# Optimization experiments

Hardware: AMD Instinct MI355X
Metric: run time of the kernel (lower is better)

## Reference

```python
import jax, jax.numpy as jnp
import numpy as np

N = 100000      # nodes
E = 1600000     # edges (avg degree 16)
IN = 128        # in_channels
H = 128         # hidden_channels
EPS = 1e-5      # BatchNorm eps


def setup_inputs() -> dict:
    key = jax.random.key(0)
    ks = jax.random.split(key, 10)
    x = jax.random.normal(ks[0], (N, IN), jnp.float32)
    edge_index = jax.random.randint(ks[1], (2, E), 0, N, dtype=jnp.int32)

    def lin(k, i, o):
        return jax.random.normal(k, (i, o), jnp.float32) * (1.0 / np.sqrt(i))

    d2 = 2 * H
    return {
        "x": x, "edge_index": edge_index,
        # SAGEConv 1: 128 -> 128
        "w1l": lin(ks[2], IN, H), "w1r": lin(ks[3], IN, H), "b1": jnp.zeros((H,), jnp.float32),
        "g1": jnp.ones((H,), jnp.float32), "be1": jnp.zeros((H,), jnp.float32),
        "m1": jnp.zeros((H,), jnp.float32), "v1": jnp.ones((H,), jnp.float32),
        # SAGEConv 2: 128 -> 256
        "w2l": lin(ks[4], H, d2), "w2r": lin(ks[5], H, d2), "b2": jnp.zeros((d2,), jnp.float32),
        "g2": jnp.ones((d2,), jnp.float32), "be2": jnp.zeros((d2,), jnp.float32),
        "m2": jnp.zeros((d2,), jnp.float32), "v2": jnp.ones((d2,), jnp.float32),
        # SAGEConv 3: 256 -> 256
        "w3l": lin(ks[6], d2, d2), "w3r": lin(ks[7], d2, d2), "b3": jnp.zeros((d2,), jnp.float32),
        "g3": jnp.ones((d2,), jnp.float32), "be3": jnp.zeros((d2,), jnp.float32),
        "m3": jnp.zeros((d2,), jnp.float32), "v3": jnp.ones((d2,), jnp.float32),
    }


def _sage_conv(x, src, dst, wl, wr, b):
    # PyG SAGEConv (mean aggr): out = mean_{j in N(i)} x_j @ W_l + x_i @ W_r + b
    agg = jax.ops.segment_sum(x[src], dst, num_segments=N)          # [N, d_in]
    deg = jax.ops.segment_sum(jnp.ones((src.shape[0],), x.dtype), dst, num_segments=N)
    mean = agg / jnp.maximum(deg, 1.0)[:, None]
    return mean @ wl + x @ wr + b


def _bn(x, g, b, m, v):
    # BatchNorm1d in eval mode (running stats); dropout is a no-op in eval
    return (x - m) * jax.lax.rsqrt(v + EPS) * g + b


def reference(x, edge_index,
              w1l, w1r, b1, g1, be1, m1, v1,
              w2l, w2r, b2, g2, be2, m2, v2,
              w3l, w3r, b3, g3, be3, m3, v3):
    src, dst = edge_index[0], edge_index[1]
    h = _bn(jax.nn.relu(_sage_conv(x, src, dst, w1l, w1r, b1)), g1, be1, m1, v1)
    h = _bn(jax.nn.relu(_sage_conv(h, src, dst, w2l, w2r, b2)), g2, be2, m2, v2)
    h = _bn(jax.nn.relu(_sage_conv(h, src, dst, w3l, w3r, b3)), g3, be3, m3, v3)
    return h  # [N, 2*H]
```

## Files before the change

### kernel.cpp

```cpp
#include <hip/hip_runtime.h>

#define NNODES 100000
#define NEDGES 1600000
#define EPSV 1e-5f

#define NB   391
#define BCAP 4608
#define EPB  4096

typedef __attribute__((ext_vector_type(8))) short bf16x8;
typedef __attribute__((ext_vector_type(4))) float f32x4;

#if defined(__has_builtin)
#  if __has_builtin(__builtin_amdgcn_cvt_pk_f32_fp8) && __has_builtin(__builtin_amdgcn_cvt_pk_fp8_f32)
#    define HAS_FP8_CVT 1
#  endif
#endif
#ifndef HAS_FP8_CVT
#  define HAS_FP8_CVT 0
#endif

__device__ __forceinline__ ushort f2bf(float f) {
    union { float f; uint u; } c; c.f = f;
    uint u = c.u;
    return (ushort)((u + 0x7fffu + ((u >> 16) & 1u)) >> 16);
}
__device__ __forceinline__ uint pack2(float f0, float f1) {
    return (uint)f2bf(f0) | ((uint)f2bf(f1) << 16);
}

#if !HAS_FP8_CVT
__device__ __forceinline__ float fp8_dec1(uint b) {
    uint e = (b >> 3) & 0xFu, m = b & 7u, s = b >> 7;
    union { uint u; float f; } c;
    c.u = e ? ((s << 31) | ((e + 120u) << 23) | (m << 20)) : (s << 31);
    return c.f;
}
__device__ __forceinline__ uint fp8_enc1(float x) {
    union { float f; uint u; } c; c.f = x;
    uint u = c.u, s = u >> 31;
    float ax = fabsf(x);
    if (ax < 0.015625f) return s << 7;
    if (ax > 448.0f)    return (s << 7) | 0x7Eu;
    u = u + 0x7FFFFu + ((u >> 20) & 1u);
    uint e = ((u >> 23) & 0xFFu) - 120u;
    uint m = (u >> 20) & 7u;
    if (e > 15u) return (s << 7) | 0x7Eu;
    return (s << 7) | (e << 3) | m;
}
#endif

__device__ __forceinline__ void accf8(float* a, uint2 v) {
#if HAS_FP8_CVT
    auto p0 = __builtin_amdgcn_cvt_pk_f32_fp8((int)v.x, false);
    auto p1 = __builtin_amdgcn_cvt_pk_f32_fp8((int)v.x, true);
    auto p2 = __builtin_amdgcn_cvt_pk_f32_fp8((int)v.y, false);
    auto p3 = __builtin_amdgcn_cvt_pk_f32_fp8((int)v.y, true);
    a[0] += p0[0]; a[1] += p0[1]; a[2] += p1[0]; a[3] += p1[1];
    a[4] += p2[0]; a[5] += p2[1]; a[6] += p3[0]; a[7] += p3[1];
#else
    a[0] += fp8_dec1(v.x & 0xFFu);         a[1] += fp8_dec1((v.x >> 8) & 0xFFu);
    a[2] += fp8_dec1((v.x >> 16) & 0xFFu); a[3] += fp8_dec1(v.x >> 24);
    a[4] += fp8_dec1(v.y & 0xFFu);         a[5] += fp8_dec1((v.y >> 8) & 0xFFu);
    a[6] += fp8_dec1((v.y >> 16) & 0xFFu); a[7] += fp8_dec1(v.y >> 24);
#endif
}

__device__ __forceinline__ uint f2fp8(float f) {
#if HAS_FP8_CVT
    return ((uint)__builtin_amdgcn_cvt_pk_fp8_f32(f, f, 0, false)) & 0xFFu;
#else
    return fp8_enc1(f);
#endif
}

__device__ __forceinline__ uint packf8_4(float f0, float f1, float f2, float f3) {
#if HAS_FP8_CVT
    int r = 0;
    r = __builtin_amdgcn_cvt_pk_fp8_f32(f0, f1, r, false);
    r = __builtin_amdgcn_cvt_pk_fp8_f32(f2, f3, r, true);
    return (uint)r;
#else
    return fp8_enc1(f0) | (fp8_enc1(f1) << 8) | (fp8_enc1(f2) << 16) | (fp8_enc1(f3) << 24);
#endif
}

__global__ __launch_bounds__(256) void part_kernel(
    const int* __restrict__ src, const int* __restrict__ dst,
    int* __restrict__ cursor, uint2* __restrict__ pairs, int E)
{
    __shared__ int lcnt[NB];
    __shared__ int lbase[NB];
    const int t = threadIdx.x;
    for (int i = t; i < NB; i += 256) lcnt[i] = 0;
    __syncthreads();

    const int base = blockIdx.x * EPB;
    const int lim  = min(base + EPB, E);

    for (int e = base + t; e < lim; e += 256)
        atomicAdd(&lcnt[((unsigned)dst[e]) >> 8], 1);
    __syncthreads();

    for (int i = t; i < NB; i += 256) {
        int c = lcnt[i];
        lbase[i] = c ? atomicAdd(&cursor[i], c) : 0;
        lcnt[i] = 0;
    }
    __syncthreads();

    for (int e = base + t; e < lim; e += 256) {
        int d = dst[e];
        int b = ((unsigned)d) >> 8;
        int p = lbase[b] + atomicAdd(&lcnt[b], 1);
        if (p < BCAP) pairs[(size_t)b * BCAP + p] = make_uint2((uint)src[e], (uint)d);
    }
}

__global__ __launch_bounds__(512) void bscan_kernel(const int* __restrict__ cursor,
                                                    int* __restrict__ colBase)
{
    __shared__ int s[512];
    int t = threadIdx.x;
    int v = (t < NB) ? min(cursor[t], BCAP) : 0;
    s[t] = v;
    __syncthreads();
    #pragma unroll
    for (int off = 1; off < 512; off <<= 1) {
        int a = (t >= off) ? s[t - off] : 0;
        __syncthreads();
        s[t] += a;
        __syncthreads();
    }
    if (t < NB) colBase[t] = s[t] - v;
}

__global__ __launch_bounds__(256) void csr_fin_kernel(
    const uint2* __restrict__ pairs, const int* __restrict__ cursor,
    const int* __restrict__ colBase, int* __restrict__ cnt,
    int* __restrict__ rptr, int* __restrict__ col, int n)
{
    __shared__ int lcnt[256];
    __shared__ int lofs[256];
    const int b = blockIdx.x;
    const int t = threadIdx.x;
    const int ecnt  = min(cursor[b], BCAP);
    const int cbase = colBase[b];
    const uint2* __restrict__ pp = pairs + (size_t)b * BCAP;

    lcnt[t] = 0;
    __syncthreads();
    for (int e = t; e < ecnt; e += 256)
        atomicAdd(&lcnt[pp[e].y & 255u], 1);
    __syncthreads();

    const int v = lcnt[t];
    lofs[t] = v;
    __syncthreads();
    #pragma unroll
    for (int off = 1; off < 256; off <<= 1) {
        int a = (t >= off) ? lofs[t - off] : 0;
        __syncthreads();
        lofs[t] += a;
        __syncthreads();
    }
    const int excl = lofs[t] - v;

    const int node = (b << 8) + t;
    if (node < n) {
        cnt[node]  = v;
        rptr[node] = cbase + excl + v;
    }
    __syncthreads();
    lcnt[t] = excl;
    __syncthreads();

    for (int e = t; e < ecnt; e += 256) {
        uint2 pr = pp[e];
        int p = cbase + atomicAdd(&lcnt[pr.y & 255u], 1);
        col[p] = (int)pr.x;
    }
}

__global__ void cvt_x_kernel(const float* __restrict__ in, ushort* __restrict__ outb,
                             unsigned char* __restrict__ out8, int n4) {
    int i = blockIdx.x * blockDim.x + threadIdx.x;
    if (i < n4) {
        float4 v = ((const float4*)in)[i];
        ushort4 o;
        o.x = f2bf(v.x); o.y = f2bf(v.y); o.z = f2bf(v.z); o.w = f2bf(v.w);
        ((ushort4*)outb)[i] = o;
        ((uint*)out8)[i] = packf8_4(v.x, v.y, v.z, v.w);
    }
}

__global__ void wT_all_kernel(
    const float* __restrict__ w1l, const float* __restrict__ w1r,
    const float* __restrict__ w2l, const float* __restrict__ w2r,
    const float* __restrict__ w3l, const float* __restrict__ w3r,
    ushort* __restrict__ t1l, ushort* __restrict__ t1r,
    ushort* __restrict__ t2l, ushort* __restrict__ t2r,
    ushort* __restrict__ t3l, ushort* __restrict__ t3r)
{
    int idx = blockIdx.x * blockDim.x + threadIdx.x;
    const float* w; ushort* wt; int K, Nout, i;
    if      (idx <  16384) { w = w1l; wt = t1l; K = 128; Nout = 128; i = idx; }
    else if (idx <  32768) { w = w1r; wt = t1r; K = 128; Nout = 128; i = idx - 16384; }
    else if (idx <  65536) { w = w2l; wt = t2l; K = 128; Nout = 256; i = idx - 32768; }
    else if (idx <  98304) { w = w2r; wt = t2r; K = 128; Nout = 256; i = idx - 65536; }
    else if (idx < 163840) { w = w3l; wt = t3l; K = 256; Nout = 256; i = idx - 98304; }
    else if (idx < 229376) { w = w3r; wt = t3r; K = 256; Nout = 256; i = idx - 163840; }
    else return;
    int k = i / Nout, n = i - k * Nout;
    wt[(size_t)n * K + k] = f2bf(w[i]);
}

template<int D>
__global__ __launch_bounds__(256) void gather_f8(
    const unsigned char* __restrict__ x, const int* __restrict__ rptr,
    const int* __restrict__ cnt, const int* __restrict__ col,
    ushort* __restrict__ agg, int n)
{
    constexpr int TPN = D / 8;
    constexpr int NPB = 256 / TPN;
    const int node = blockIdx.x * NPB + threadIdx.x / TPN;
    const int lane = threadIdx.x % TPN;
    if (node >= n) return;

    const int c   = cnt[node];
    const int end = rptr[node];
    const uint2* __restrict__ xp = (const uint2*)x + lane;

    float a[8] = {};
    int e = end - c;
    for (; e + 7 < end; e += 8) {
        int s0 = col[e],     s1 = col[e + 1], s2 = col[e + 2], s3 = col[e + 3];
        int s4 = col[e + 4], s5 = col[e + 5], s6 = col[e + 6], s7 = col[e + 7];
        uint2 v0 = xp[(size_t)s0 * TPN];
        uint2 v1 = xp[(size_t)s1 * TPN];
        uint2 v2 = xp[(size_t)s2 * TPN];
        uint2 v3 = xp[(size_t)s3 * TPN];
        uint2 v4 = xp[(size_t)s4 * TPN];
        uint2 v5 = xp[(size_t)s5 * TPN];
        uint2 v6 = xp[(size_t)s6 * TPN];
        uint2 v7 = xp[(size_t)s7 * TPN];
        accf8(a, v0); accf8(a, v1); accf8(a, v2); accf8(a, v3);
        accf8(a, v4); accf8(a, v5); accf8(a, v6); accf8(a, v7);
    }
    for (; e + 1 < end; e += 2) {
        uint2 v0 = xp[(size_t)col[e] * TPN];
        uint2 v1 = xp[(size_t)col[e + 1] * TPN];
        accf8(a, v0); accf8(a, v1);
    }
    if (e < end) accf8(a, xp[(size_t)col[e] * TPN]);

    const float inv = 1.0f / fmaxf((float)c, 1.0f);
    uint4 o;
    o.x = pack2(a[0] * inv, a[1] * inv);
    o.y = pack2(a[2] * inv, a[3] * inv);
    o.z = pack2(a[4] * inv, a[5] * inv);
    o.w = pack2(a[6] * inv, a[7] * inv);
    ((uint4*)agg)[(size_t)node * TPN + lane] = o;
}

template<int DIN, int DOUT, bool OUTF32, bool WRITE8>
__global__ __launch_bounds__(256) void mfma_layer(
    const ushort* __restrict__ xin, const ushort* __restrict__ agg,
    const ushort* __restrict__ wlT, const ushort* __restrict__ wrT,
    const float* __restrict__ bias, const float* __restrict__ gamma,
    const float* __restrict__ beta, const float* __restrict__ rmean,
    const float* __restrict__ rvar, void* __restrict__ outp,
    unsigned char* __restrict__ out8, int M)
{
    constexpr int BM = 128, BN = 128, BK = 32;
    constexpr int LDA = BK + 8;
    __shared__ ushort As[BM * LDA];
    __shared__ ushort Bs[BN * LDA];

    const int tid  = threadIdx.x;
    const int lane = tid & 63;
    const int wid  = tid >> 6;
    const int wm   = (wid & 1) * 64;
    const int wn   = (wid >> 1) * 64;
    const int lr   = lane & 15;
    const int quad = lane >> 4;

    const int row0 = blockIdx.x * BM;
    const int col0 = blockIdx.y * BN;

    f32x4 acc[4][4] = {};

    const int s_row  = tid >> 2;
    const int s_koff = (tid & 3) * 8;

    #pragma unroll
    for (int phase = 0; phase < 2; ++phase) {
        const ushort* __restrict__ A = phase ? xin : agg;
        const ushort* __restrict__ W = phase ? wrT : wlT;

        for (int k0 = 0; k0 < DIN; k0 += BK) {
            int gr0 = row0 + s_row;       gr0 = gr0 < M ? gr0 : M - 1;
            int gr1 = row0 + s_row + 64;  gr1 = gr1 < M ? gr1 : M - 1;
            uint4 a0v = *(const uint4*)(A + (size_t)gr0 * DIN + k0 + s_koff);
            uint4 a1v = *(const uint4*)(A + (size_t)gr1 * DIN + k0 + s_koff);
            uint4 b0v = *(const uint4*)(W + (size_t)(col0 + s_row) * DIN + k0 + s_koff);
            uint4 b1v = *(const uint4*)(W + (size_t)(col0 + s_row + 64) * DIN + k0 + s_koff);

            __syncthreads();
            *(uint4*)&As[s_row * LDA + s_koff]        = a0v;
            *(uint4*)&As[(s_row + 64) * LDA + s_koff] = a1v;
            *(uint4*)&Bs[s_row * LDA + s_koff]        = b0v;
            *(uint4*)&Bs[(s_row + 64) * LDA + s_koff] = b1v;
            __syncthreads();

            bf16x8 af[4], bf[4];
            #pragma unroll
            for (int t = 0; t < 4; ++t) {
                af[t] = *(const bf16x8*)&As[(wm + t * 16 + lr) * LDA + quad * 8];
                bf[t] = *(const bf16x8*)&Bs[(wn + t * 16 + lr) * LDA + quad * 8];
            }
            #pragma unroll
            for (int mt = 0; mt < 4; ++mt)
                #pragma unroll
                for (int nt = 0; nt < 4; ++nt)
                    acc[mt][nt] = __builtin_amdgcn_mfma_f32_16x16x32_bf16(
                        af[mt], bf[nt], acc[mt][nt], 0, 0, 0);
        }
    }

    float bj[4], sj[4], mj[4], bej[4];
    #pragma unroll
    for (int nt = 0; nt < 4; ++nt) {
        int gc = col0 + wn + nt * 16 + lr;
        bj[nt]  = bias[gc];
        sj[nt]  = rsqrtf(rvar[gc] + EPSV) * gamma[gc];
        mj[nt]  = rmean[gc];
        bej[nt] = beta[gc];
    }
    #pragma unroll
    for (int mt = 0; mt < 4; ++mt) {
        #pragma unroll
        for (int r = 0; r < 4; ++r) {
            int grow = row0 + wm + mt * 16 + quad * 4 + r;
            if (grow < M) {
                #pragma unroll
                for (int nt = 0; nt < 4; ++nt) {
                    int gc = col0 + wn + nt * 16 + lr;
                    float h = acc[mt][nt][r] + bj[nt];
                    h = fmaxf(h, 0.0f);
                    h = (h - mj[nt]) * sj[nt] + bej[nt];
                    if (OUTF32) ((float*)outp)[(size_t)grow * DOUT + gc] = h;
                    else        ((ushort*)outp)[(size_t)grow * DOUT + gc] = f2bf(h);
                    if (WRITE8) out8[(size_t)grow * DOUT + gc] = (unsigned char)f2fp8(h);
                }
            }
        }
    }
}

extern "C" void kernel_launch(void* const* d_in, const int* in_sizes, int n_in,
                              void* d_out, int out_size, void* d_ws, size_t ws_size,
                              hipStream_t stream) {
    const int N = NNODES;
    const int E = NEDGES;

    const float* x   = (const float*)d_in[0];
    const int*   ei  = (const int*)d_in[1];
    const int*   src = ei;
    const int*   dst = ei + E;

    const float* w1l = (const float*)d_in[2];
    const float* w1r = (const float*)d_in[3];
    const float* b1  = (const float*)d_in[4];
    const float* g1  = (const float*)d_in[5];
    const float* be1 = (const float*)d_in[6];
    const float* m1  = (const float*)d_in[7];
    const float* v1  = (const float*)d_in[8];

    const float* w2l = (const float*)d_in[9];
    const float* w2r = (const float*)d_in[10];
    const float* b2  = (const float*)d_in[11];
    const float* g2  = (const float*)d_in[12];
    const float* be2 = (const float*)d_in[13];
    const float* m2  = (const float*)d_in[14];
    const float* v2  = (const float*)d_in[15];

    const float* w3l = (const float*)d_in[16];
    const float* w3r = (const float*)d_in[17];
    const float* b3  = (const float*)d_in[18];
    const float* g3  = (const float*)d_in[19];
    const float* be3 = (const float*)d_in[20];
    const float* m3  = (const float*)d_in[21];
    const float* v3  = (const float*)d_in[22];

    float* out = (float*)d_out;

    char*   wp      = (char*)d_ws;
    int*    cnt     = (int*)wp;     wp += (size_t)N * sizeof(int);
    int*    rptr    = (int*)wp;     wp += (size_t)N * sizeof(int);
    int*    cursor  = (int*)wp;     wp += 512 * sizeof(int);
    int*    colBase = (int*)wp;     wp += 512 * sizeof(int);
    int*    col     = (int*)wp;     wp += (size_t)E * sizeof(int);
    uint2*  pairs   = (uint2*)wp;   wp += (size_t)NB * BCAP * sizeof(uint2);
    ushort* xbf     = (ushort*)wp;  wp += (size_t)N * 128 * sizeof(ushort);
    ushort* h1      = (ushort*)wp;  wp += (size_t)N * 128 * sizeof(ushort);
    ushort* h2      = (ushort*)wp;  wp += (size_t)N * 256 * sizeof(ushort);
    ushort* aggb    = (ushort*)wp;  wp += (size_t)N * 256 * sizeof(ushort);
    unsigned char* h2f8 = (unsigned char*)wp; wp += (size_t)N * 256;
    ushort* w1lT    = (ushort*)wp;  wp += 128 * 128 * sizeof(ushort);
    ushort* w1rT    = (ushort*)wp;  wp += 128 * 128 * sizeof(ushort);
    ushort* w2lT    = (ushort*)wp;  wp += 256 * 128 * sizeof(ushort);
    ushort* w2rT    = (ushort*)wp;  wp += 256 * 128 * sizeof(ushort);
    ushort* w3lT    = (ushort*)wp;  wp += 256 * 256 * sizeof(ushort);
    ushort* w3rT    = (ushort*)wp;

    unsigned char* xf8  = (unsigned char*)pairs;
    unsigned char* h1f8 = (unsigned char*)pairs;

    const int T = 256;

    hipMemsetAsync(cursor, 0, 512 * sizeof(int), stream);
    part_kernel<<<(E + EPB - 1) / EPB, 256, 0, stream>>>(src, dst, cursor, pairs, E);
    bscan_kernel<<<1, 512, 0, stream>>>(cursor, colBase);
    csr_fin_kernel<<<NB, 256, 0, stream>>>(pairs, cursor, colBase, cnt, rptr, col, N);

    cvt_x_kernel<<<((N * 128 / 4) + T - 1) / T, T, 0, stream>>>(x, xbf, xf8, N * 128 / 4);
    wT_all_kernel<<<229376 / 256, 256, 0, stream>>>(w1l, w1r, w2l, w2r, w3l, w3r,
                                                    w1lT, w1rT, w2lT, w2rT, w3lT, w3rT);

    const dim3 g1g((N + 127) / 128, 1);
    const dim3 g2g((N + 127) / 128, 2);

    gather_f8<128><<<(N + 15) / 16, 256, 0, stream>>>(xf8, rptr, cnt, col, aggb, N);
    mfma_layer<128, 128, false, true><<<g1g, 256, 0, stream>>>(
        xbf, aggb, w1lT, w1rT, b1, g1, be1, m1, v1, h1, h1f8, N);

    gather_f8<128><<<(N + 15) / 16, 256, 0, stream>>>(h1f8, rptr, cnt, col, aggb, N);
    mfma_layer<128, 256, false, true><<<g2g, 256, 0, stream>>>(
        h1, aggb, w2lT, w2rT, b2, g2, be2, m2, v2, h2, h2f8, N);

    gather_f8<256><<<(N + 7) / 8, 256, 0, stream>>>(h2f8, rptr, cnt, col, aggb, N);
    mfma_layer<256, 256, true, false><<<g2g, 256, 0, stream>>>(
        h2, aggb, w3lT, w3rT, b3, g3, be3, m3, v3, out, nullptr, N);
}
```

Measured before the change: 491.5 us.

## Use direct global-to-LDS loads with XOR-swizzled tiles and BK=64 in MFMA GEMM

The GEMM tile loader now uses global_load_lds (direct global-to-shared DMA) instead of staging through registers. The padded LDS layout is replaced by an XOR-swizzled unpadded layout, and the K step doubles to 64 with two MFMA sub-steps per tile. The grid is flattened to 1D so column tiles of the same row block are adjacent, which should improve L2 reuse of A rows. This removes register staging and halves the barriers per K, at the cost of a less obvious swizzle and reliance on the LDS-DMA builtin's per-lane address semantics.

```diff
diff --git a/kernel.cpp b/kernel.cpp
--- a/kernel.cpp
+++ b/kernel.cpp
@@ -83,6 +83,13 @@
 #else
     return fp8_enc1(f0) | (fp8_enc1(f1) << 8) | (fp8_enc1(f2) << 16) | (fp8_enc1(f3) << 24);
 #endif
+}
+
+__device__ __forceinline__ void load_lds16(const ushort* g, ushort* l) {
+    __builtin_amdgcn_global_load_lds(
+        (const __attribute__((address_space(1))) void*)g,
+        (__attribute__((address_space(3))) void*)l,
+        16, 0, 0);
 }
 
 __global__ __launch_bounds__(256) void part_kernel(
@@ -272,10 +279,10 @@
     const float* __restrict__ rvar, void* __restrict__ outp,
     unsigned char* __restrict__ out8, int M)
 {
-    constexpr int BM = 128, BN = 128, BK = 32;
-    constexpr int LDA = BK + 8;
-    __shared__ ushort As[BM * LDA];
-    __shared__ ushort Bs[BN * LDA];
+    constexpr int BM = 128, BN = 128, BK = 64;
+    constexpr int NBY = DOUT / BN;
+    __shared__ ushort As[BM * BK];
+    __shared__ ushort Bs[BN * BK];
 
     const int tid  = threadIdx.x;
     const int lane = tid & 63;
@@ -285,13 +292,13 @@
     const int lr   = lane & 15;
     const int quad = lane >> 4;
 
-    const int row0 = blockIdx.x * BM;
-    const int col0 = blockIdx.y * BN;
+    const int row0 = (blockIdx.x / NBY) * BM;
+    const int col0 = (blockIdx.x % NBY) * BN;
 
     f32x4 acc[4][4] = {};
 
-    const int s_row  = tid >> 2;
-    const int s_koff = (tid & 3) * 8;
+    const int srow = tid >> 3;
+    const int schk = (tid & 7) ^ (srow & 7);
 
     #pragma unroll
     for (int phase = 0; phase < 2; ++phase) {
@@ -299,32 +306,37 @@
         const ushort* __restrict__ W = phase ? wrT : wlT;
 
         for (int k0 = 0; k0 < DIN; k0 += BK) {
-            int gr0 = row0 + s_row;       gr0 = gr0 < M ? gr0 : M - 1;
-            int gr1 = row0 + s_row + 64;  gr1 = gr1 < M ? gr1 : M - 1;
-            uint4 a0v = *(const uint4*)(A + (size_t)gr0 * DIN + k0 + s_koff);
-            uint4 a1v = *(const uint4*)(A + (size_t)gr1 * DIN + k0 + s_koff);
-            uint4 b0v = *(const uint4*)(W + (size_t)(col0 + s_row) * DIN + k0 + s_koff);
-            uint4 b1v = *(const uint4*)(W + (size_t)(col0 + s_row + 64) * DIN + k0 + s_koff);
-
             __syncthreads();
-            *(uint4*)&As[s_row * LDA + s_koff]        = a0v;
-            *(uint4*)&As[(s_row + 64) * LDA + s_koff] = a1v;
-            *(uint4*)&Bs[s_row * LDA + s_koff]        = b0v;
-            *(uint4*)&Bs[(s_row + 64) * LDA + s_koff] = b1v;
+            #pragma unroll
+            for (int r = 0; r < 4; ++r) {
+                const int row = srow + r * 32;
+                int gra = row0 + row; gra = gra < M ? gra : M - 1;
+                load_lds16(A + (size_t)gra * DIN + k0 + schk * 8,
+                           &As[(r * 256 + tid) * 8]);
+                load_lds16(W + (size_t)(col0 + row) * DIN + k0 + schk * 8,
+                           &Bs[(r * 256 + tid) * 8]);
+            }
             __syncthreads();
 
-            bf16x8 af[4], bf[4];
             #pragma unroll
-            for (int t = 0; t < 4; ++t) {
-                af[t] = *(const bf16x8*)&As[(wm + t * 16 + lr) * LDA + quad * 8];
-                bf[t] = *(const bf16x8*)&Bs[(wn + t * 16 + lr) * LDA + quad * 8];
+            for (int sub = 0; sub < 2; ++sub) {
+                bf16x8 af[4], bf[4];
+                #pragma unroll
+                for (int t = 0; t < 4; ++t) {
+                    const int ra = wm + t * 16 + lr;
+                    const int rb = wn + t * 16 + lr;
+                    const int ca = ((sub << 2) | quad) ^ (ra & 7);
+                    const int cb = ((sub << 2) | quad) ^ (rb & 7);
+                    af[t] = *(const bf16x8*)&As[ra * BK + ca * 8];
+                    bf[t] = *(const bf16x8*)&Bs[rb * BK + cb * 8];
+                }
+                #pragma unroll
+                for (int mt = 0; mt < 4; ++mt)
+                    #pragma unroll
+                    for (int nt = 0; nt < 4; ++nt)
+                        acc[mt][nt] = __builtin_amdgcn_mfma_f32_16x16x32_bf16(
+                            af[mt], bf[nt], acc[mt][nt], 0, 0, 0);
             }
-            #pragma unroll
-            for (int mt = 0; mt < 4; ++mt)
-                #pragma unroll
-                for (int nt = 0; nt < 4; ++nt)
-                    acc[mt][nt] = __builtin_amdgcn_mfma_f32_16x16x32_bf16(
-                        af[mt], bf[nt], acc[mt][nt], 0, 0, 0);
         }
     }
 
@@ -428,18 +440,17 @@
     wT_all_kernel<<<229376 / 256, 256, 0, stream>>>(w1l, w1r, w2l, w2r, w3l, w3r,
                                                     w1lT, w1rT, w2lT, w2rT, w3lT, w3rT);
 
-    const dim3 g1g((N + 127) / 128, 1);
-    const dim3 g2g((N + 127) / 128, 2);
+    const int nrb = (N + 127) / 128;
 
     gather_f8<128><<<(N + 15) / 16, 256, 0, stream>>>(xf8, rptr, cnt, col, aggb, N);
-    mfma_layer<128, 128, false, true><<<g1g, 256, 0, stream>>>(
+    mfma_layer<128, 128, false, true><<<nrb * 1, 256, 0, stream>>>(
         xbf, aggb, w1lT, w1rT, b1, g1, be1, m1, v1, h1, h1f8, N);
 
     gather_f8<128><<<(N + 15) / 16, 256, 0, stream>>>(h1f8, rptr, cnt, col, aggb, N);
-    mfma_layer<128, 256, false, true><<<g2g, 256, 0, stream>>>(
+    mfma_layer<128, 256, false, true><<<nrb * 2, 256, 0, stream>>>(
         h1, aggb, w2lT, w2rT, b2, g2, be2, m2, v2, h2, h2f8, N);
 
     gather_f8<256><<<(N + 7) / 8, 256, 0, stream>>>(h2f8, rptr, cnt, col, aggb, N);
-    mfma_layer<256, 256, true, false><<<g2g, 256, 0, stream>>>(
+    mfma_layer<256, 256, true, false><<<nrb * 2, 256, 0, stream>>>(
         h2, aggb, w3lT, w3rT, b3, g3, be3, m3, v3, out, nullptr, N);
 }
```

Result: no change. 485.0 us (-1.3%).
